# Kernel optimization log

Measured on AMD Instinct MI355X. Metric: run time of the kernel, lower is better.

## Reference

```python
import jax, jax.numpy as jnp
import numpy as np

T, N, F, H, C, E = 8, 50000, 128, 64, 4, 800000


def setup_inputs() -> dict:
    key = jax.random.key(0)
    ks = jax.random.split(key, 8)
    x = jax.random.normal(ks[0], (T, N, F), jnp.float32)
    edges = jax.random.randint(ks[1], (T, 2, E), 0, N, jnp.int32)
    # GCNConv weights (one per timestep, glorot-ish scale) + Linear layers
    Wg = jax.random.normal(ks[2], (T, F, H), jnp.float32) / np.sqrt(F)
    bg = jnp.zeros((T, H), jnp.float32)
    W1 = jax.random.normal(ks[3], (H, 32), jnp.float32) / np.sqrt(H)
    b1 = jnp.zeros((32,), jnp.float32)
    W2 = jax.random.normal(ks[4], (32, 16), jnp.float32) / np.sqrt(32)
    b2 = jnp.zeros((16,), jnp.float32)
    W3 = jax.random.normal(ks[5], (16, C), jnp.float32) / np.sqrt(16)
    b3 = jnp.zeros((C,), jnp.float32)
    return dict(x=x, edges=edges, Wg=Wg, bg=bg, W1=W1, b1=b1, W2=W2, b2=b2, W3=W3, b3=b3)


def gcn_conv(x, edge_index, W, b):
    """PyG GCNConv: add self-loops, sym-normalized aggregation of x @ W, plus bias."""
    n = x.shape[0]
    loop = jnp.arange(n, dtype=edge_index.dtype)
    src = jnp.concatenate([edge_index[0], loop])  # message sources
    dst = jnp.concatenate([edge_index[1], loop])  # aggregation targets
    deg = jax.ops.segment_sum(jnp.ones_like(dst, dtype=x.dtype), dst, num_segments=n)
    dinv = jnp.where(deg > 0, jax.lax.rsqrt(deg), 0.0)
    xw = x @ W                                    # [n, H]
    norm = (dinv[src] * dinv[dst])[:, None]       # [E+n, 1]
    out = jax.ops.segment_sum(xw[src] * norm, dst, num_segments=n)
    return out + b


def reference(x, edges, Wg, bg, W1, b1, W2, b2, W3, b3):
    def step(acc, inp):
        xt, et, Wt, bt = inp
        return acc + jax.nn.relu(gcn_conv(xt, et, Wt, bt)), None

    acc0 = jnp.zeros((x.shape[1], Wg.shape[-1]), x.dtype)
    h, _ = jax.lax.scan(step, acc0, (x, edges, Wg, bg))  # sum over T timesteps
    h = jax.nn.relu(h)                 # dropout omitted (eval mode)
    h = jax.nn.relu(h @ W1 + b1)
    h = jax.nn.relu(h @ W2 + b2)
    logits = h @ W3 + b3
    return jax.nn.log_softmax(logits, axis=1)
```

## Files before the change

### kernel.cpp

```cpp
#include <hip/hip_runtime.h>
#include <hip/hip_bf16.h>

#define TT 8
#define NN 50000
#define FF 128
#define HH 64
#define CC 4
#define EE 800000
#define NB2 391
#define CAP 2560
#define BPT 64

typedef unsigned short u16;
typedef unsigned int u32;
typedef __attribute__((ext_vector_type(8))) short bf16x8;
typedef __attribute__((ext_vector_type(4))) float f32x4;

static __device__ __forceinline__ float bflo(u32 w) {
    union { unsigned int i; float f; } v; v.i = w << 16; return v.f;
}
static __device__ __forceinline__ float bfhi(u32 w) {
    union { unsigned int i; float f; } v; v.i = w & 0xFFFF0000u; return v.f;
}
static __device__ __forceinline__ u16 cvt_bf16(float f) {
    __hip_bfloat16 b = __float2bfloat16(f);
    return *reinterpret_cast<u16*>(&b);
}

__global__ __launch_bounds__(256) void multisplit_kernel(const int* __restrict__ edges,
                                                         int* __restrict__ gcur, u32* __restrict__ binned) {
    __shared__ u32 sbuf[NB2][16];
    __shared__ int scnt[NB2];
    int bid = blockIdx.x;
    int t = bid & 7;
    int blk = bid >> 3;
    const int per = (EE + BPT - 1) / BPT;
    int e0 = blk * per;
    int e1 = e0 + per; if (e1 > EE) e1 = EE;

    for (int i = threadIdx.x; i < NB2; i += 256) scnt[i] = 0;
    __syncthreads();

    const int* es = edges + (size_t)(t * 2 + 0) * EE;
    const int* ed = edges + (size_t)(t * 2 + 1) * EE;
    int* gc = gcur + t * NB2;
    u32* bb = binned + (size_t)t * NB2 * CAP;

    for (int base = e0; base < e1; base += 512) {
        u32 recA = 0, recB = 0; int bA = -1, bB = -1;
        int eA = base + threadIdx.x;
        int eB = base + 256 + threadIdx.x;
        if (eA < e1) {
            int src = es[eA], dst = ed[eA];
            bA = dst >> 7;
            recA = (u32)src | ((u32)(dst & 127) << 16);
            int p = atomicAdd(&scnt[bA], 1);
            if (p < 16) { sbuf[bA][p] = recA; bA = -1; }
        }
        if (eB < e1) {
            int src = es[eB], dst = ed[eB];
            bB = dst >> 7;
            recB = (u32)src | ((u32)(dst & 127) << 16);
            int p = atomicAdd(&scnt[bB], 1);
            if (p < 16) { sbuf[bB][p] = recB; bB = -1; }
        }
        __syncthreads();
        for (int fb = threadIdx.x; fb < NB2; fb += 256) {
            if (scnt[fb] >= 16) {
                int g = atomicAdd(&gc[fb], 16);
                uint4* dp = (uint4*)(bb + (size_t)fb * CAP + g);
                uint4* sp = (uint4*)&sbuf[fb][0];
                dp[0] = sp[0]; dp[1] = sp[1]; dp[2] = sp[2]; dp[3] = sp[3];
                scnt[fb] = 0;
            }
        }
        __syncthreads();
        if (bA >= 0) {
            int p = atomicAdd(&scnt[bA], 1);
            if (p < 16) sbuf[bA][p] = recA;
            else { int g = atomicAdd(&gc[bA], 1); bb[(size_t)bA * CAP + g] = recA; }
        }
        if (bB >= 0) {
            int p = atomicAdd(&scnt[bB], 1);
            if (p < 16) sbuf[bB][p] = recB;
            else { int g = atomicAdd(&gc[bB], 1); bb[(size_t)bB * CAP + g] = recB; }
        }
        __syncthreads();
    }
    for (int fb = threadIdx.x; fb < NB2; fb += 256) {
        int c = scnt[fb];
        if (c > 0) {
            int g = atomicAdd(&gc[fb], c);
            for (int k = 0; k < c; ++k) bb[(size_t)fb * CAP + g + k] = sbuf[fb][k];
        }
    }
}

__global__ __launch_bounds__(256) void csr_scatter_kernel(const u32* __restrict__ binned, const int* __restrict__ gcur,
                                                          u16* __restrict__ srclist, u32* __restrict__ nodeinfo,
                                                          float* __restrict__ dinv) {
    __shared__ u32 recs[CAP];
    __shared__ int hist[128];
    __shared__ int cur[128];
    int b = blockIdx.x, t = blockIdx.y, tid = threadIdx.x;
    int node0 = b * 128;
    int tot = gcur[t * NB2 + b];
    const u32* win = binned + ((size_t)t * NB2 + b) * CAP;

    for (int i = tid; i < tot; i += 256) recs[i] = win[i];
    if (tid < 128) hist[tid] = 0;
    __syncthreads();
    for (int i = tid; i < tot; i += 256) atomicAdd(&hist[recs[i] >> 16], 1);
    __syncthreads();
    int h = 0;
    if (tid < 128) h = hist[tid];
    for (int off = 1; off < 128; off <<= 1) {
        int v = 0;
        if (tid < 128 && tid >= off) v = hist[tid - off];
        __syncthreads();
        if (tid < 128) hist[tid] += v;
        __syncthreads();
    }
    if (tid < 128) {
        int excl = hist[tid] - h;
        cur[tid] = excl;
        int node = node0 + tid;
        if (node < NN) {
            nodeinfo[t * NN + node] = (u32)(b * CAP + excl) | ((u32)h << 20);
            dinv[t * NN + node] = rsqrtf(1.0f + (float)h);
        }
    }
    __syncthreads();
    u16* sl = srclist + (size_t)t * NB2 * CAP;
    for (int i = tid; i < tot; i += 256) {
        u32 rec = recs[i];
        int d = rec >> 16;
        int p = atomicAdd(&cur[d], 1);
        sl[(size_t)b * CAP + p] = (u16)(rec & 0xFFFF);
    }
}

__global__ __launch_bounds__(256) void wt_prep_kernel(const float* __restrict__ Wg, u16* __restrict__ wt) {
    int t = blockIdx.x;
    const float* w = Wg + t * FF * HH;
    u16* o = wt + (size_t)t * HH * FF;
    for (int i = threadIdx.x; i < FF * HH; i += 256) {
        int k = i >> 6, c = i & 63;
        o[c * FF + k] = cvt_bf16(w[i]);
    }
}

__global__ __launch_bounds__(256) void xw_kernel(const float* __restrict__ x, const u16* __restrict__ wt,
                                                 const float* __restrict__ dinv, u16* __restrict__ y) {
    int t = blockIdx.y;
    int row0 = blockIdx.x * 64;
    int tid = threadIdx.x;
    int w = tid >> 6, lane = tid & 63;
    int wr = w * 16;
    int l15 = lane & 15, lg = lane >> 4;
    int arow = row0 + wr + l15;
    const float* xt = x + (size_t)t * NN * FF;
    const u16* wtt = wt + (size_t)t * HH * FF;

    f32x4 d[4] = {{0,0,0,0},{0,0,0,0},{0,0,0,0},{0,0,0,0}};
    #pragma unroll
    for (int k0 = 0; k0 < 128; k0 += 32) {
        int kb = k0 + lg * 8;
        union { bf16x8 v; __hip_bfloat162 h[4]; } au;
        if (arow < NN) {
            float4 f0 = *reinterpret_cast<const float4*>(&xt[(size_t)arow * FF + kb]);
            float4 f1 = *reinterpret_cast<const float4*>(&xt[(size_t)arow * FF + kb + 4]);
            au.h[0] = __float22bfloat162_rn(make_float2(f0.x, f0.y));
            au.h[1] = __float22bfloat162_rn(make_float2(f0.z, f0.w));
            au.h[2] = __float22bfloat162_rn(make_float2(f1.x, f1.y));
            au.h[3] = __float22bfloat162_rn(make_float2(f1.z, f1.w));
        } else {
            au.v = (bf16x8){0,0,0,0,0,0,0,0};
        }
        #pragma unroll
        for (int n = 0; n < 4; ++n) {
            bf16x8 bf = *reinterpret_cast<const bf16x8*>(&wtt[(size_t)(n * 16 + l15) * FF + kb]);
            d[n] = __builtin_amdgcn_mfma_f32_16x16x32_bf16(au.v, bf, d[n], 0, 0, 0);
        }
    }
    int rbase = row0 + wr + lg * 4;
    float dv[4];
    #pragma unroll
    for (int i = 0; i < 4; ++i) {
        int grow = rbase + i;
        dv[i] = (grow < NN) ? dinv[t * NN + grow] : 0.f;
    }
    u16* yt = y + (size_t)t * NN * HH;
    #pragma unroll
    for (int n = 0; n < 4; ++n) {
        int col = n * 16 + l15;
        #pragma unroll
        for (int i = 0; i < 4; ++i) {
            int grow = rbase + i;
            if (grow < NN) yt[(size_t)grow * HH + col] = cvt_bf16(d[n][i] * dv[i]);
        }
    }
}

__global__ __launch_bounds__(256) void agg_kernel(const u16* __restrict__ y, const float* __restrict__ dinv,
                                                  const u32* __restrict__ nodeinfo, const u16* __restrict__ srclist,
                                                  const float* __restrict__ bg, float* __restrict__ acc) {
    int node = blockIdx.x * 4 + (threadIdx.x >> 6);
    int lane = threadIdx.x & 63;
    int sub = lane >> 4;
    int fo = lane & 15;
    float a0 = 0.f, a1 = 0.f, a2 = 0.f, a3 = 0.f;
    for (int t = 0; t < TT; ++t) {
        const u16* yt = y + (size_t)t * NN * HH;
        u32 info = nodeinfo[t * NN + node];
        int cnt = info >> 20;
        const u16* sl = srclist + (size_t)t * NB2 * CAP + (info & 0xFFFFF);
        float s0 = 0.f, s1 = 0.f, s2 = 0.f, s3 = 0.f;
        int j = 0;
        for (; j + 16 <= cnt; j += 16) {
            int e0 = sl[j + sub], e1 = sl[j + 4 + sub], e2 = sl[j + 8 + sub], e3 = sl[j + 12 + sub];
            uint2 v0 = *reinterpret_cast<const uint2*>(&yt[(size_t)e0 * HH + fo * 4]);
            uint2 v1 = *reinterpret_cast<const uint2*>(&yt[(size_t)e1 * HH + fo * 4]);
            uint2 v2 = *reinterpret_cast<const uint2*>(&yt[(size_t)e2 * HH + fo * 4]);
            uint2 v3 = *reinterpret_cast<const uint2*>(&yt[(size_t)e3 * HH + fo * 4]);
            s0 += (bflo(v0.x) + bflo(v1.x)) + (bflo(v2.x) + bflo(v3.x));
            s1 += (bfhi(v0.x) + bfhi(v1.x)) + (bfhi(v2.x) + bfhi(v3.x));
            s2 += (bflo(v0.y) + bflo(v1.y)) + (bflo(v2.y) + bflo(v3.y));
            s3 += (bfhi(v0.y) + bfhi(v1.y)) + (bfhi(v2.y) + bfhi(v3.y));
        }
        for (; j < cnt; j += 4) {
            int e = j + sub;
            uint2 v = make_uint2(0u, 0u);
            if (e < cnt) {
                int srcid = sl[e];
                v = *reinterpret_cast<const uint2*>(&yt[(size_t)srcid * HH + fo * 4]);
            }
            s0 += bflo(v.x);
            s1 += bfhi(v.x);
            s2 += bflo(v.y);
            s3 += bfhi(v.y);
        }
        s0 += __shfl_xor(s0, 16, 64); s0 += __shfl_xor(s0, 32, 64);
        s1 += __shfl_xor(s1, 16, 64); s1 += __shfl_xor(s1, 32, 64);
        s2 += __shfl_xor(s2, 16, 64); s2 += __shfl_xor(s2, 32, 64);
        s3 += __shfl_xor(s3, 16, 64); s3 += __shfl_xor(s3, 32, 64);
        uint2 sv = *reinterpret_cast<const uint2*>(&yt[(size_t)node * HH + fo * 4]);
        s0 += bflo(sv.x);
        s1 += bfhi(sv.x);
        s2 += bflo(sv.y);
        s3 += bfhi(sv.y);
        float dvv = dinv[t * NN + node];
        float4 bgv = *reinterpret_cast<const float4*>(&bg[t * HH + fo * 4]);
        a0 += fmaxf(dvv * s0 + bgv.x, 0.f);
        a1 += fmaxf(dvv * s1 + bgv.y, 0.f);
        a2 += fmaxf(dvv * s2 + bgv.z, 0.f);
        a3 += fmaxf(dvv * s3 + bgv.w, 0.f);
    }
    if (sub == 0) {
        float4 o = make_float4(a0, a1, a2, a3);
        *reinterpret_cast<float4*>(&acc[(size_t)node * HH + fo * 4]) = o;
    }
}

__global__ __launch_bounds__(256) void head_kernel(const float* __restrict__ acc,
                                                   const float* __restrict__ W1, const float* __restrict__ b1,
                                                   const float* __restrict__ W2, const float* __restrict__ b2,
                                                   const float* __restrict__ W3, const float* __restrict__ b3,
                                                   float* __restrict__ out) {
    __shared__ float w1[64 * 32], w2[32 * 16], w3[16 * 4], bb1[32], bb2[16], bb3[4];
    int tid = threadIdx.x;
    for (int i = tid; i < 2048; i += 256) w1[i] = W1[i];
    for (int i = tid; i < 512; i += 256) w2[i] = W2[i];
    if (tid < 64) w3[tid] = W3[tid];
    if (tid < 32) bb1[tid] = b1[tid];
    if (tid < 16) bb2[tid] = b2[tid];
    if (tid < 4) bb3[tid] = b3[tid];
    __syncthreads();
    int node = blockIdx.x * 256 + tid;
    if (node >= NN) return;

    float a[64];
    #pragma unroll
    for (int k = 0; k < 64; ++k) a[k] = acc[(size_t)node * HH + k];

    float h1[32];
    for (int j = 0; j < 32; ++j) {
        float s = bb1[j];
        #pragma unroll
        for (int k = 0; k < 64; ++k) s += a[k] * w1[k * 32 + j];
        h1[j] = fmaxf(s, 0.f);
    }
    float h2[16];
    for (int j = 0; j < 16; ++j) {
        float s = bb2[j];
        #pragma unroll
        for (int k = 0; k < 32; ++k) s += h1[k] * w2[k * 16 + j];
        h2[j] = fmaxf(s, 0.f);
    }
    float l[4];
    for (int c = 0; c < 4; ++c) {
        float s = bb3[c];
        #pragma unroll
        for (int k = 0; k < 16; ++k) s += h2[k] * w3[k * 4 + c];
        l[c] = s;
    }
    float m = fmaxf(fmaxf(l[0], l[1]), fmaxf(l[2], l[3]));
    float sum = 0.f;
    #pragma unroll
    for (int c = 0; c < 4; ++c) sum += expf(l[c] - m);
    float lse = logf(sum);
    float4 o;
    o.x = l[0] - m - lse; o.y = l[1] - m - lse; o.z = l[2] - m - lse; o.w = l[3] - m - lse;
    *reinterpret_cast<float4*>(&out[(size_t)node * CC]) = o;
}

extern "C" void kernel_launch(void* const* d_in, const int* in_sizes, int n_in,
                              void* d_out, int out_size, void* d_ws, size_t ws_size,
                              hipStream_t stream) {
    const float* x    = (const float*)d_in[0];
    const int*  edges = (const int*)d_in[1];
    const float* Wg   = (const float*)d_in[2];
    const float* bg   = (const float*)d_in[3];
    const float* W1   = (const float*)d_in[4];
    const float* b1   = (const float*)d_in[5];
    const float* W2   = (const float*)d_in[6];
    const float* b2   = (const float*)d_in[7];
    const float* W3   = (const float*)d_in[8];
    const float* b3   = (const float*)d_in[9];
    float* out = (float*)d_out;

    char* ws = (char*)d_ws;
    size_t o = 0;
    int* gcur      = (int*)(ws + o); o += (size_t)TT * NB2 * 4;
    o = (o + 255) & ~(size_t)255;
    float* dinv    = (float*)(ws + o); o += (size_t)TT * NN * 4;
    u32* nodeinfo  = (u32*)(ws + o); o += (size_t)TT * NN * 4;
    o = (o + 255) & ~(size_t)255;
    u16* wt        = (u16*)(ws + o); o += (size_t)TT * HH * FF * 2;
    o = (o + 255) & ~(size_t)255;
    u32* binned    = (u32*)(ws + o); o += (size_t)TT * NB2 * CAP * 4;
    u16* srclist   = (u16*)(ws + o); o += (size_t)TT * NB2 * CAP * 2;
    u16* y         = (u16*)(ws + o); o += (size_t)TT * NN * HH * 2;
    float* acc     = (float*)(ws + o); o += (size_t)NN * HH * 4;

    hipMemsetAsync(gcur, 0, (size_t)TT * NB2 * 4, stream);

    multisplit_kernel<<<BPT * TT, 256, 0, stream>>>(edges, gcur, binned);

    dim3 gsc(NB2, TT);
    csr_scatter_kernel<<<gsc, 256, 0, stream>>>(binned, gcur, srclist, nodeinfo, dinv);

    wt_prep_kernel<<<TT, 256, 0, stream>>>(Wg, wt);

    dim3 gx(782, TT);
    xw_kernel<<<gx, 256, 0, stream>>>(x, wt, dinv, y);

    agg_kernel<<<12500, 256, 0, stream>>>(y, dinv, nodeinfo, srclist, bg, acc);

    head_kernel<<<196, 256, 0, stream>>>(acc, W1, b1, W2, b2, W3, b3, out);
}
```

Baseline: 391.0 us.

## Stage xw output through LDS for coalesced 16-byte stores and double rows per block

The xw kernel now computes 128 rows per block, two 16-row MFMA tiles per wave, so each B-fragment load from the weight matrix is reused twice. Results go through a padded shared-memory tile and are written to global memory as coalesced 16-byte stores instead of scattered 2-byte stores. This targets write inefficiency and redundant weight loads, at the cost of more LDS, an extra barrier and half as many blocks.

```diff
diff --git a/kernel.cpp b/kernel.cpp
--- a/kernel.cpp
+++ b/kernel.cpp
@@ -153,52 +153,68 @@
 __global__ __launch_bounds__(256) void xw_kernel(const float* __restrict__ x, const u16* __restrict__ wt,
                                                  const float* __restrict__ dinv, u16* __restrict__ y) {
     int t = blockIdx.y;
-    int row0 = blockIdx.x * 64;
+    int row0 = blockIdx.x * 128;
     int tid = threadIdx.x;
     int w = tid >> 6, lane = tid & 63;
-    int wr = w * 16;
     int l15 = lane & 15, lg = lane >> 4;
-    int arow = row0 + wr + l15;
+    __shared__ __align__(16) u16 ylds[128][72];
     const float* xt = x + (size_t)t * NN * FF;
     const u16* wtt = wt + (size_t)t * HH * FF;
 
-    f32x4 d[4] = {{0,0,0,0},{0,0,0,0},{0,0,0,0},{0,0,0,0}};
+    f32x4 d[2][4] = {{{0,0,0,0},{0,0,0,0},{0,0,0,0},{0,0,0,0}},
+                     {{0,0,0,0},{0,0,0,0},{0,0,0,0},{0,0,0,0}}};
     #pragma unroll
     for (int k0 = 0; k0 < 128; k0 += 32) {
         int kb = k0 + lg * 8;
-        union { bf16x8 v; __hip_bfloat162 h[4]; } au;
-        if (arow < NN) {
-            float4 f0 = *reinterpret_cast<const float4*>(&xt[(size_t)arow * FF + kb]);
-            float4 f1 = *reinterpret_cast<const float4*>(&xt[(size_t)arow * FF + kb + 4]);
-            au.h[0] = __float22bfloat162_rn(make_float2(f0.x, f0.y));
-            au.h[1] = __float22bfloat162_rn(make_float2(f0.z, f0.w));
-            au.h[2] = __float22bfloat162_rn(make_float2(f1.x, f1.y));
-            au.h[3] = __float22bfloat162_rn(make_float2(f1.z, f1.w));
-        } else {
-            au.v = (bf16x8){0,0,0,0,0,0,0,0};
+        union { bf16x8 v; __hip_bfloat162 h[4]; } au[2];
+        #pragma unroll
+        for (int s = 0; s < 2; ++s) {
+            int arow = row0 + w * 32 + s * 16 + l15;
+            if (arow < NN) {
+                float4 f0 = *reinterpret_cast<const float4*>(&xt[(size_t)arow * FF + kb]);
+                float4 f1 = *reinterpret_cast<const float4*>(&xt[(size_t)arow * FF + kb + 4]);
+                au[s].h[0] = __float22bfloat162_rn(make_float2(f0.x, f0.y));
+                au[s].h[1] = __float22bfloat162_rn(make_float2(f0.z, f0.w));
+                au[s].h[2] = __float22bfloat162_rn(make_float2(f1.x, f1.y));
+                au[s].h[3] = __float22bfloat162_rn(make_float2(f1.z, f1.w));
+            } else {
+                au[s].v = (bf16x8){0,0,0,0,0,0,0,0};
+            }
         }
         #pragma unroll
         for (int n = 0; n < 4; ++n) {
             bf16x8 bf = *reinterpret_cast<const bf16x8*>(&wtt[(size_t)(n * 16 + l15) * FF + kb]);
-            d[n] = __builtin_amdgcn_mfma_f32_16x16x32_bf16(au.v, bf, d[n], 0, 0, 0);
-        }
-    }
-    int rbase = row0 + wr + lg * 4;
-    float dv[4];
-    #pragma unroll
-    for (int i = 0; i < 4; ++i) {
-        int grow = rbase + i;
-        dv[i] = (grow < NN) ? dinv[t * NN + grow] : 0.f;
-    }
+            d[0][n] = __builtin_amdgcn_mfma_f32_16x16x32_bf16(au[0].v, bf, d[0][n], 0, 0, 0);
+            d[1][n] = __builtin_amdgcn_mfma_f32_16x16x32_bf16(au[1].v, bf, d[1][n], 0, 0, 0);
+        }
+    }
+    #pragma unroll
+    for (int s = 0; s < 2; ++s) {
+        int rl = w * 32 + s * 16 + lg * 4;
+        float dv[4];
+        #pragma unroll
+        for (int i = 0; i < 4; ++i) {
+            int grow = row0 + rl + i;
+            dv[i] = (grow < NN) ? dinv[t * NN + grow] : 0.f;
+        }
+        #pragma unroll
+        for (int n = 0; n < 4; ++n) {
+            int col = n * 16 + l15;
+            #pragma unroll
+            for (int i = 0; i < 4; ++i)
+                ylds[rl + i][col] = cvt_bf16(d[s][n][i] * dv[i]);
+        }
+    }
+    __syncthreads();
     u16* yt = y + (size_t)t * NN * HH;
     #pragma unroll
-    for (int n = 0; n < 4; ++n) {
-        int col = n * 16 + l15;
-        #pragma unroll
-        for (int i = 0; i < 4; ++i) {
-            int grow = rbase + i;
-            if (grow < NN) yt[(size_t)grow * HH + col] = cvt_bf16(d[n][i] * dv[i]);
-        }
+    for (int it = 0; it < 4; ++it) {
+        int idx = it * 256 + tid;
+        int r = idx >> 3, c8 = (idx & 7) * 8;
+        int grow = row0 + r;
+        if (grow < NN)
+            *reinterpret_cast<uint4*>(&yt[(size_t)grow * HH + c8]) =
+                *reinterpret_cast<const uint4*>(&ylds[r][c8]);
     }
 }
 
@@ -352,7 +368,7 @@
 
     wt_prep_kernel<<<TT, 256, 0, stream>>>(Wg, wt);
 
-    dim3 gx(782, TT);
+    dim3 gx(NB2, TT);
     xw_kernel<<<gx, 256, 0, stream>>>(x, wt, dinv, y);
 
     agg_kernel<<<12500, 256, 0, stream>>>(y, dinv, nodeinfo, srclist, bg, acc);
```

After: 366.9 us. -6.2%, faster.
